# Kernel optimization log

Hardware: AMD Instinct MI355X
Metric: run time of the kernel (lower is better)

## Reference

```python
import jax, jax.numpy as jnp
import numpy as np

B, T, Z, X, R, HT, HO = 512, 256, 128, 64, 1024, 1024, 1024


def _linear(x, w, b):
    return x @ w.T + b


def _loc_scale(x, p):
    # p = (gate_ih_w, gate_ih_b, gate_hz_w, gate_hz_b,
    #      prop_ih_w, prop_ih_b, prop_hz_w, prop_hz_b,
    #      loc_w, loc_b, scale_w, scale_b)
    (g_ih_w, g_ih_b, g_hz_w, g_hz_b,
     p_ih_w, p_ih_b, p_hz_w, p_hz_b,
     l_w, l_b, s_w, s_b) = p
    gate = jax.nn.sigmoid(_linear(jax.nn.relu(_linear(x, g_ih_w, g_ih_b)), g_hz_w, g_hz_b))
    proposed = _linear(jax.nn.relu(_linear(x, p_ih_w, p_ih_b)), p_hz_w, p_hz_b)
    loc = (1.0 - gate) * _linear(x, l_w, l_b) + gate * proposed
    scale = jax.nn.softplus(_linear(jax.nn.relu(proposed), s_w, s_b))
    return loc, scale


def _gru_cell(x, h, w_ih, b_ih, w_hh, b_hh):
    # torch GRUCell: gates ordered (r, z, n)
    gi = x @ w_ih.T + b_ih
    gh = h @ w_hh.T + b_hh
    i_r, i_z, i_n = jnp.split(gi, 3, axis=-1)
    h_r, h_z, h_n = jnp.split(gh, 3, axis=-1)
    r = jax.nn.sigmoid(i_r + h_r)
    z = jax.nn.sigmoid(i_z + h_z)
    n = jnp.tanh(i_n + r * h_n)
    return (1.0 - z) * n + z * h


def _mk_linear(key, out_dim, in_dim, std=0.02):
    kw, kb = jax.random.split(key)
    w = jax.random.normal(kw, (out_dim, in_dim), jnp.float32) * std
    b = jnp.zeros((out_dim,), jnp.float32)
    return w, b


def setup_inputs() -> dict:
    key = jax.random.key(0)
    ks = jax.random.split(key, 20)
    inp = {}
    inp['mini_batch'] = jax.random.normal(ks[0], (B, T, X), jnp.float32)
    inp['eps'] = jax.random.normal(ks[1], (B, T, Z), jnp.float32)
    inp['z_0'] = jnp.zeros((Z,), jnp.float32)
    inp['h_0'] = jnp.zeros((R,), jnp.float32)
    # GRUCell params
    inp['gru_w_ih'], inp['gru_b_ih'] = _mk_linear(ks[2], 3 * R, Z)
    inp['gru_w_hh'], inp['gru_b_hh'] = _mk_linear(ks[3], 3 * R, R)
    # trans LocScaleTransformer: in=R, out=Z, hidden=HT
    inp['t_gate_ih_w'], inp['t_gate_ih_b'] = _mk_linear(ks[4], HT, R)
    inp['t_gate_hz_w'], inp['t_gate_hz_b'] = _mk_linear(ks[5], Z, HT)
    inp['t_prop_ih_w'], inp['t_prop_ih_b'] = _mk_linear(ks[6], HT, R)
    inp['t_prop_hz_w'], inp['t_prop_hz_b'] = _mk_linear(ks[7], Z, HT)
    inp['t_loc_w'], inp['t_loc_b'] = _mk_linear(ks[8], Z, R)
    inp['t_scale_w'], inp['t_scale_b'] = _mk_linear(ks[9], Z, Z)
    # obs LocScaleTransformer: in=Z, out=X, hidden=HO
    inp['o_gate_ih_w'], inp['o_gate_ih_b'] = _mk_linear(ks[10], HO, Z)
    inp['o_gate_hz_w'], inp['o_gate_hz_b'] = _mk_linear(ks[11], X, HO)
    inp['o_prop_ih_w'], inp['o_prop_ih_b'] = _mk_linear(ks[12], HO, Z)
    inp['o_prop_hz_w'], inp['o_prop_hz_b'] = _mk_linear(ks[13], X, HO)
    inp['o_loc_w'], inp['o_loc_b'] = _mk_linear(ks[14], X, Z)
    inp['o_scale_w'], inp['o_scale_b'] = _mk_linear(ks[15], X, X)
    return inp


def reference(mini_batch, eps, z_0, h_0,
              gru_w_ih, gru_b_ih, gru_w_hh, gru_b_hh,
              t_gate_ih_w, t_gate_ih_b, t_gate_hz_w, t_gate_hz_b,
              t_prop_ih_w, t_prop_ih_b, t_prop_hz_w, t_prop_hz_b,
              t_loc_w, t_loc_b, t_scale_w, t_scale_b,
              o_gate_ih_w, o_gate_ih_b, o_gate_hz_w, o_gate_hz_b,
              o_prop_ih_w, o_prop_ih_b, o_prop_hz_w, o_prop_hz_b,
              o_loc_w, o_loc_b, o_scale_w, o_scale_b):
    b = mini_batch.shape[0]
    trans_p = (t_gate_ih_w, t_gate_ih_b, t_gate_hz_w, t_gate_hz_b,
               t_prop_ih_w, t_prop_ih_b, t_prop_hz_w, t_prop_hz_b,
               t_loc_w, t_loc_b, t_scale_w, t_scale_b)
    obs_p = (o_gate_ih_w, o_gate_ih_b, o_gate_hz_w, o_gate_hz_b,
             o_prop_ih_w, o_prop_ih_b, o_prop_hz_w, o_prop_hz_b,
             o_loc_w, o_loc_b, o_scale_w, o_scale_b)

    z_prev = jnp.broadcast_to(z_0, (b, z_0.shape[0]))
    h_prev = jnp.broadcast_to(h_0, (b, h_0.shape[0]))

    def step(carry, eps_t):
        z_p, h_p = carry
        rnn_out = _gru_cell(z_p, h_p, gru_w_ih, gru_b_ih, gru_w_hh, gru_b_hh)
        z_loc, z_scale = _loc_scale(rnn_out, trans_p)
        z_t = z_loc + z_scale * eps_t  # reparameterized Normal sample
        x_loc, x_scale = _loc_scale(z_t, obs_p)
        return (z_t, rnn_out), jnp.concatenate([x_loc, x_scale], axis=-1)

    # scan over time: eps -> [T, B, Z]
    _, out = jax.lax.scan(step, (z_prev, h_prev), eps.transpose(1, 0, 2))
    return out.transpose(1, 0, 2)  # [B, T, 2*X]
```

## Files before the change

kernel.cpp:

```cpp
#include <hip/hip_runtime.h>
#include <math.h>


typedef unsigned short u16;
typedef unsigned long long u64;
typedef __bf16 bf16x8 __attribute__((ext_vector_type(8)));
typedef u16    u16x8  __attribute__((ext_vector_type(8)));
typedef float  f32x4  __attribute__((ext_vector_type(4)));

#define DI __device__ __forceinline__
#define LDS_STRIDE 72

DI u16  f2b(float f){ union{float f; unsigned u;} c; c.f = f;
                      return (u16)((c.u + 0x7fffu + ((c.u>>16)&1u))>>16); }
DI float b2f(u16 x){ union{unsigned u; float f;} c; c.u = ((unsigned)x)<<16; return c.f; }
DI float sigm (float x){ return 1.f/(1.f+expf(-x)); }
DI float softp(float x){ return (x>15.f)? x : log1pf(expf(x)); }

DI f32x4 mfma16(bf16x8 a, bf16x8 b, f32x4 c){
  return __builtin_amdgcn_mfma_f32_16x16x32_bf16(a,b,c,0,0,0);
}
DI bf16x8 ldw8b(const u16* __restrict__ g){
  return __builtin_bit_cast(bf16x8, *(const u16x8*)g);
}
DI bf16x8 ldfragS(const u16* l, int row, int ko, int stride){
  return __builtin_bit_cast(bf16x8, *(const u16x8*)(l + row*stride + ko));
}
DI bf16x8 ldfrag(const u16* l, int row, int ko){ return ldfragS(l, row, ko, LDS_STRIDE); }

DI u64 ldc64(const void* p){
  return __hip_atomic_load((const u64*)p, __ATOMIC_RELAXED, __HIP_MEMORY_SCOPE_AGENT);
}
DI u16x8 ldc128(const u16* g){
  union{u64 q[2]; u16x8 v;} u; u.q[0] = ldc64(g); u.q[1] = ldc64(g + 4); return u.v;
}
DI u16 ldc16(const u16* p){
  return __hip_atomic_load(p, __ATOMIC_RELAXED, __HIP_MEMORY_SCOPE_AGENT);
}
DI void stc16(u16* p, u16 v){
  __hip_atomic_store(p, v, __ATOMIC_RELAXED, __HIP_MEMORY_SCOPE_AGENT);
}
DI float ldc32f(const float* p){
  unsigned u = __hip_atomic_load((const unsigned*)p, __ATOMIC_RELAXED, __HIP_MEMORY_SCOPE_AGENT);
  union{unsigned u; float f;} c; c.u = u; return c.f;
}
DI void stc32f(float* p, float v){
  union{float f; unsigned u;} c; c.f = v;
  __hip_atomic_store((unsigned*)p, c.u, __ATOMIC_RELAXED, __HIP_MEMORY_SCOPE_AGENT);
}

DI void gsync(unsigned* bar, unsigned bi, int blk){
  __syncthreads();
  if(threadIdx.x == 0){
    unsigned v = __hip_atomic_fetch_add(bar + (blk & 7)*32, 1u,
                   __ATOMIC_RELAXED, __HIP_MEMORY_SCOPE_AGENT);
    if(v == bi*64u + 63u){
      unsigned r = __hip_atomic_fetch_add(bar + 256, 1u,
                     __ATOMIC_RELAXED, __HIP_MEMORY_SCOPE_AGENT);
      if(r == bi*8u + 7u)
        __hip_atomic_store(bar + 288, bi + 1u,
                           __ATOMIC_RELAXED, __HIP_MEMORY_SCOPE_AGENT);
    }
    while(__hip_atomic_load(bar + 288, __ATOMIC_RELAXED,
                            __HIP_MEMORY_SCOPE_AGENT) <= bi)
      __builtin_amdgcn_s_sleep(4);
  }
  asm volatile("" ::: "memory");
  __syncthreads();
}

__global__ __launch_bounds__(256) void k_cvt(const float* __restrict__ s,
                                             u16* __restrict__ d){
  int i = (blockIdx.x*256 + threadIdx.x)*8;
  f32x4 p0 = *(const f32x4*)(s+i), p1 = *(const f32x4*)(s+i+4);
  u16x8 o;
  o[0]=f2b(p0[0]); o[1]=f2b(p0[1]); o[2]=f2b(p0[2]); o[3]=f2b(p0[3]);
  o[4]=f2b(p1[0]); o[5]=f2b(p1[1]); o[6]=f2b(p1[2]); o[7]=f2b(p1[3]);
  *(u16x8*)(d+i) = o;
}

__global__ __launch_bounds__(256) void k_init(u16* __restrict__ hb,
                                              u16* __restrict__ zb,
                                              const float* __restrict__ h0,
                                              const float* __restrict__ z0){
  int idx = blockIdx.x*256 + threadIdx.x;
  hb[idx] = f2b(h0[idx & 1023]);
  if(idx < 512*128) zb[idx] = f2b(z0[idx & 127]);
}

__global__ void k_bzero(unsigned* b){ b[threadIdx.x] = 0u; b[threadIdx.x+256] = 0u; }

struct SeqP {
  const float *eps, *h0, *z0;
  const float *gbih, *gbhh, *tgb, *tpb, *tlb, *tghzb, *tphzb, *tsb;
  const u16 *wih, *whh, *tgw, *tpw, *tlw, *tghzw, *tphzw, *tsw;
  float *out, *GP;
  u16 *Hbuf, *hb16, *zb16;
  unsigned *bar;
};

DI void mlp_tile(const u16* __restrict__ A,
                 const u16* __restrict__ W,
                 const float* __restrict__ bias, int act,
                 u16* __restrict__ Cb,
                 u16* smem, int tid)
{
  const int lane=tid&63, w=tid>>6, l16=lane&15, quad=lane>>4, wm=w>>1, wn=w&1;
  const int ar=tid>>3, ac=(tid&7)*8, br=tid>>2, bc=(tid&3)*16;
  f32x4 acc[2] = {};
  u16x8 a0,a1,a2,a3,u0,u1,u2,u3,v0,v1,v2,v3;
#define MT_ISSUE(ra,ru,rv,is) do{ \
    ra = ldc128(A + (size_t)ar*1024 + (is)*64 + ac); \
    ru = *(const u16x8*)(W + (size_t)br*1024 + (is)*64 + bc); \
    rv = *(const u16x8*)(W + (size_t)br*1024 + (is)*64 + bc + 8); \
  }while(0)
#define MT_STEP(ra,ru,rv,it,nx) do{ \
    u16* b_ = smem + ((it)&1)*6912; \
    *(u16x8*)(b_ + ar*LDS_STRIDE + ac) = ra; \
    *(u16x8*)(b_ + 2304 + br*LDS_STRIDE + bc) = ru; \
    *(u16x8*)(b_ + 2304 + br*LDS_STRIDE + bc + 8) = rv; \
    asm volatile("s_waitcnt lgkmcnt(0)" ::: "memory"); \
    __builtin_amdgcn_s_barrier(); \
    __builtin_amdgcn_sched_barrier(0); \
    if((nx) < 16) MT_ISSUE(ra,ru,rv,(nx)); \
    _Pragma("unroll") \
    for(int kc=0;kc<2;kc++){ \
      int ko = kc*32 + quad*8; \
      bf16x8 aa = ldfrag(b_, wm*16 + l16, ko); \
      bf16x8 q0 = ldfrag(b_ + 2304, wn*32 + l16, ko); \
      bf16x8 q1 = ldfrag(b_ + 2304, wn*32 + 16 + l16, ko); \
      acc[0] = mfma16(aa,q0,acc[0]); \
      acc[1] = mfma16(aa,q1,acc[1]); \
    } \
  }while(0)
  MT_ISSUE(a0,u0,v0,0); MT_ISSUE(a1,u1,v1,1);
  MT_ISSUE(a2,u2,v2,2); MT_ISSUE(a3,u3,v3,3);
#pragma unroll 1
  for(int ib=0; ib<16; ib+=4){
    MT_STEP(a0,u0,v0, ib+0, ib+4);
    MT_STEP(a1,u1,v1, ib+1, ib+5);
    MT_STEP(a2,u2,v2, ib+2, ib+6);
    MT_STEP(a3,u3,v3, ib+3, ib+7);
  }
#undef MT_ISSUE
#undef MT_STEP
  __syncthreads();
#pragma unroll
  for(int nf=0; nf<2; nf++)
#pragma unroll
  for(int i=0; i<4; i++){
    int m  = wm*16 + quad*4 + i;
    int cl = wn*32 + nf*16 + l16;
    float v = acc[nf][i] + bias[cl];
    if(act) v = fmaxf(v, 0.f);
    stc16(&Cb[(size_t)m*2176 + cl], f2b(v));
  }
}

__global__ __launch_bounds__(256, 2) void k_seq(SeqP p)
{
  __shared__ u16 smem[18432];
  const int blk  = blockIdx.x;
  const int tid  = threadIdx.x;
  const int lane = tid & 63, w = tid >> 6;
  const int l16  = lane & 15, quad = lane >> 4;
  const int wm   = w >> 1, wn = w & 1;
  const int ar   = tid >> 3, ac = (tid & 7) * 8;

  const int p1m0 = (blk >> 5) * 32;
  const int p1n0 = (blk & 31) * 32;
  const int p1n  = p1n0 + wn*16 + l16;
  f32x4 hreg;
  { float h0v = p.h0[p1n]; hreg[0]=h0v; hreg[1]=h0v; hreg[2]=h0v; hreg[3]=h0v; }

  unsigned bi = 0;

#pragma unroll 1
  for(int t = 0; t < 256; t++){
    const u16* hbi = p.hb16 + (size_t)(t&1)*524288;
    u16*       hbo = p.hb16 + (size_t)((t+1)&1)*524288;

    {
      f32x4 acc[4] = {};
      u16x8 a0,a1,a2, w00,w01,w02, w10,w11,w12, w20,w21,w22;
#define P1_ISSUE(ra,r0,r1,r2,is) do{ \
      const u16 *A_, *W_; int ld_, k0_; \
      if((is) < 2){ A_ = p.zb16 + (size_t)p1m0*128;  W_ = p.wih; ld_=128;  k0_=(is)*64; } \
      else        { A_ = hbi    + (size_t)p1m0*1024; W_ = p.whh; ld_=1024; k0_=((is)-2)*64; } \
      ra = ldc128(A_ + (size_t)ar*ld_ + k0_ + ac); \
      r0 = *(const u16x8*)(W_ + (size_t)(p1n0 + ar)*ld_        + k0_ + ac); \
      r1 = *(const u16x8*)(W_ + (size_t)(1024 + p1n0 + ar)*ld_ + k0_ + ac); \
      r2 = *(const u16x8*)(W_ + (size_t)(2048 + p1n0 + ar)*ld_ + k0_ + ac); \
    }while(0)
#define P1_STEP(ra,r0,r1,r2,it,nx) do{ \
      u16* b_ = smem + ((it)&1)*9216; \
      *(u16x8*)(b_ + ar*LDS_STRIDE + ac) = ra; \
      *(u16x8*)(b_ + 2304 + ar*LDS_STRIDE + ac) = r0; \
      *(u16x8*)(b_ + 4608 + ar*LDS_STRIDE + ac) = r1; \
      *(u16x8*)(b_ + 6912 + ar*LDS_STRIDE + ac) = r2; \
      asm volatile("s_waitcnt lgkmcnt(0)" ::: "memory"); \
      __builtin_amdgcn_s_barrier(); \
      __builtin_amdgcn_sched_barrier(0); \
      if((nx) < 18) P1_ISSUE(ra,r0,r1,r2,(nx)); \
      const int ai3_ = ((it) < 2) ? 2 : 3; \
      _Pragma("unroll") \
      for(int kc=0;kc<2;kc++){ \
        int ko = kc*32 + quad*8; \
        bf16x8 aa  = ldfrag(b_, wm*16 + l16, ko); \
        bf16x8 b0v = ldfrag(b_ + 2304, wn*16 + l16, ko); \
        bf16x8 b1v = ldfrag(b_ + 4608, wn*16 + l16, ko); \
        bf16x8 b2v = ldfrag(b_ + 6912, wn*16 + l16, ko); \
        acc[0]    = mfma16(aa,b0v,acc[0]); \
        acc[1]    = mfma16(aa,b1v,acc[1]); \
        acc[ai3_] = mfma16(aa,b2v,acc[ai3_]); \
      } \
    }while(0)
      P1_ISSUE(a0,w00,w01,w02,0);
      P1_ISSUE(a1,w10,w11,w12,1);
      P1_ISSUE(a2,w20,w21,w22,2);
#pragma unroll 1
      for(int ib=0; ib<18; ib+=3){
        P1_STEP(a0,w00,w01,w02, ib+0, ib+3);
        P1_STEP(a1,w10,w11,w12, ib+1, ib+4);
        P1_STEP(a2,w20,w21,w22, ib+2, ib+5);
      }
#undef P1_ISSUE
#undef P1_STEP
      __syncthreads();
#pragma unroll
      for(int i=0; i<4; i++){
        int m = p1m0 + wm*16 + quad*4 + i;
        int n = p1n;
        float r  = sigm (acc[0][i] + p.gbih[n]      + p.gbhh[n]);
        float z  = sigm (acc[1][i] + p.gbih[n+1024] + p.gbhh[n+1024]);
        float nn = tanhf(acc[2][i] + p.gbih[n+2048]
                         + r*(acc[3][i] + p.gbhh[n+2048]));
        float hv = (1.f-z)*nn + z*hreg[i];
        hreg[i] = hv;
        stc16(&hbo[(size_t)m*1024 + n], f2b(hv));
      }
    }
    gsync(p.bar, bi++, blk);

    {
      const int m0 = (blk >> 5) * 32;
      const int n0 = (blk & 31) * 64;
      const u16* W; const float* bias;
      if(n0 < 1024){ W = p.tgw + (size_t)n0*1024;        bias = p.tgb + n0; }
      else         { W = p.tpw + (size_t)(n0-1024)*1024; bias = p.tpb + (n0-1024); }
      mlp_tile(hbo + (size_t)m0*1024, W, bias, 1,
               p.Hbuf + (size_t)m0*2176 + n0, smem, tid);
    }
    gsync(p.bar, bi++, blk);

    if(blk < 128){
      const int m0 = (blk >> 3) * 32, n0 = (blk & 7) * 32;
      const int reg1 = (n0 >= 128);
      const u16*  A = p.Hbuf + (size_t)m0*2176 + (reg1 ? 1024 : 0);
      const u16*  W = reg1 ? p.tphzw + (size_t)(n0-128)*1024
                           : p.tghzw + (size_t)n0*1024;
      const float* bias = reg1 ? p.tphzb + (n0-128) : p.tghzb + n0;
      f32x4 acc3 = {};
      u16x8 a0,a1,a2,a3, q0,q1,q2,q3;
#define P3_ISSUE(ra,rw,is) do{ \
      ra = ldc128(A + (size_t)ar*2176 + (is)*64 + ac); \
      rw = *(const u16x8*)(W + (size_t)ar*1024 + (is)*64 + ac); \
    }while(0)
#define P3_STEP(ra,rw,it,nx) do{ \
      u16* b_ = smem + ((it)&1)*4608; \
      *(u16x8*)(b_ + ar*LDS_STRIDE + ac) = ra; \
      *(u16x8*)(b_ + 2304 + ar*LDS_STRIDE + ac) = rw; \
      asm volatile("s_waitcnt lgkmcnt(0)" ::: "memory"); \
      __builtin_amdgcn_s_barrier(); \
      __builtin_amdgcn_sched_barrier(0); \
      if((nx) < 16) P3_ISSUE(ra,rw,(nx)); \
      _Pragma("unroll") \
      for(int kc=0;kc<2;kc++){ \
        int ko = kc*32 + quad*8; \
        acc3 = mfma16(ldfrag(b_, wm*16 + l16, ko), \
                      ldfrag(b_ + 2304, wn*16 + l16, ko), acc3); \
      } \
    }while(0)
      P3_ISSUE(a0,q0,0); P3_ISSUE(a1,q1,1); P3_ISSUE(a2,q2,2); P3_ISSUE(a3,q3,3);
#pragma unroll 1
      for(int ib=0; ib<16; ib+=4){
        P3_STEP(a0,q0, ib+0, ib+4);
        P3_STEP(a1,q1, ib+1, ib+5);
        P3_STEP(a2,q2, ib+2, ib+6);
        P3_STEP(a3,q3, ib+3, ib+7);
      }
#undef P3_ISSUE
#undef P3_STEP
      __syncthreads();
#pragma unroll
      for(int i=0; i<4; i++){
        int m  = m0 + wm*16 + quad*4 + i;
        int cl = wn*16 + l16;
        stc32f(&p.GP[(size_t)m*256 + n0 + cl], acc3[i] + bias[cl]);
      }
    } else if(blk < 160){
      const int idx = blk - 128;
      const int m0  = (idx & 15) * 32;
      const int n0l = 2048 + (idx >> 4) * 64;
      mlp_tile(hbo + (size_t)m0*1024, p.tlw + (size_t)(n0l-2048)*1024,
               p.tlb + (n0l-2048), 0,
               p.Hbuf + (size_t)m0*2176 + n0l, smem, tid);
    }
    gsync(p.bar, bi++, blk);

    if(blk < 64){
      const int m0 = (blk >> 1) * 16, n0 = (blk & 1) * 64;
      u16* lp = smem;
      {
        int r = tid >> 4, c = (tid & 15) * 8;
        const float* src = p.GP + (size_t)(m0+r)*256 + 128 + c;
        union{u64 q; float f[2];} q0,q1,q2,q3;
        q0.q = ldc64(src);   q1.q = ldc64(src+2);
        q2.q = ldc64(src+4); q3.q = ldc64(src+6);
        u16x8 o;
        o[0]=f2b(fmaxf(q0.f[0],0.f)); o[1]=f2b(fmaxf(q0.f[1],0.f));
        o[2]=f2b(fmaxf(q1.f[0],0.f)); o[3]=f2b(fmaxf(q1.f[1],0.f));
        o[4]=f2b(fmaxf(q2.f[0],0.f)); o[5]=f2b(fmaxf(q2.f[1],0.f));
        o[6]=f2b(fmaxf(q3.f[0],0.f)); o[7]=f2b(fmaxf(q3.f[1],0.f));
        *(u16x8*)(lp + r*136 + c) = o;
      }
      __syncthreads();
      f32x4 acc4 = {};
      const int col = n0 + w*16 + l16;
#pragma unroll
      for(int kc=0; kc<4; kc++){
        int ko = kc*32 + quad*8;
        acc4 = mfma16(ldfragS(lp, l16, ko, 136),
                      ldw8b(p.tsw + (size_t)col*128 + ko), acc4);
      }
#pragma unroll
      for(int i=0; i<4; i++){
        int gm = m0 + quad*4 + i;
        float zs  = softp(acc4[i] + p.tsb[col]);
        float g   = sigm(ldc32f(&p.GP[(size_t)gm*256 + col]));
        float pv  = ldc32f(&p.GP[(size_t)gm*256 + 128 + col]);
        float loc = b2f(ldc16(&p.Hbuf[(size_t)gm*2176 + 2048 + col]));
        float zl  = (1.f-g)*loc + g*pv;
        float e   = p.eps[(size_t)gm*32768 + (size_t)t*128 + col];
        float zv  = zl + zs*e;
        p.out[(size_t)gm*32768 + (size_t)t*128 + col] = zv;
        stc16(&p.zb16[(size_t)gm*128 + col], f2b(zv));
      }
    }
    gsync(p.bar, bi++, blk);
  }
}

#define LH_S 520
__global__ __launch_bounds__(256) void k_obs(
  const u16* __restrict__ ogw,   const float* __restrict__ ogb,
  const u16* __restrict__ oghzw, const float* __restrict__ oghzb,
  const u16* __restrict__ opw,   const float* __restrict__ opb,
  const u16* __restrict__ ophzw, const float* __restrict__ ophzb,
  const u16* __restrict__ olw,   const float* __restrict__ olb,
  const u16* __restrict__ osw,   const float* __restrict__ osb,
  float* __restrict__ out)
{
  __shared__ u16 lz[32*136];
  __shared__ u16 lh[32*LH_S];
  __shared__ u16 lp[32*72];
  const int r0 = blockIdx.x*32;
  const int t  = r0 >> 9, b0 = r0 & 511;
  const int tid = threadIdx.x;
  const int lane = tid & 63, w = tid>>6, l16 = lane&15, quad = lane>>4;

#pragma unroll
  for(int i=0;i<2;i++){
    int ch = tid + i*256;
    int r = ch>>4, c = (ch&15)*8;
    const float* src = out + (size_t)(b0+r)*32768 + (size_t)t*128 + c;
    f32x4 p0 = *(const f32x4*)src, p1 = *(const f32x4*)(src+4);
    u16x8 o;
    o[0]=f2b(p0[0]); o[1]=f2b(p0[1]); o[2]=f2b(p0[2]); o[3]=f2b(p0[3]);
    o[4]=f2b(p1[0]); o[5]=f2b(p1[1]); o[6]=f2b(p1[2]); o[7]=f2b(p1[3]);
    *(u16x8*)(lz + r*136 + c) = o;
  }
  __syncthreads();

  f32x4 accp[2] = {}, accg[2] = {};
  const int col = w*16 + l16;

#pragma unroll 1
  for(int ph=0; ph<2; ph++){
    const u16* hw = ph ? ogw   : opw;
    const float* hb = ph ? ogb : opb;
    const u16* zw = ph ? oghzw : ophzw;
    f32x4* acc2    = ph ? accg : accp;
#pragma unroll 1
    for(int c2=0; c2<2; c2++){
      __syncthreads();
      for(int nt = w; nt < 32; nt += 4){
        int n = c2*512 + nt*16 + l16;
#pragma unroll
        for(int mi=0; mi<2; mi++){
          f32x4 a = {};
#pragma unroll
          for(int kc=0;kc<4;kc++){
            int ko = kc*32 + quad*8;
            a = mfma16(ldfragS(lz, mi*16+l16, ko, 136),
                       ldw8b(hw + (size_t)n*128 + ko), a);
          }
          float bias = hb[n];
#pragma unroll
          for(int i=0;i<4;i++)
            lh[(mi*16+quad*4+i)*LH_S + nt*16 + l16] = f2b(fmaxf(a[i]+bias, 0.f));
        }
      }
      __syncthreads();
#pragma unroll
      for(int mi=0;mi<2;mi++){
        f32x4 a = acc2[mi];
        for(int kc=0;kc<16;kc++){
          int ko = kc*32 + quad*8;
          a = mfma16(ldfragS(lh, mi*16+l16, ko, LH_S),
                     ldw8b(zw + (size_t)col*1024 + c2*512 + ko), a);
        }
        acc2[mi] = a;
      }
    }
    if(ph==0){
      float bias = ophzb[col];
#pragma unroll
      for(int mi=0;mi<2;mi++)
#pragma unroll
      for(int i=0;i<4;i++){
        float pv = accp[mi][i] + bias;
        accp[mi][i] = pv;
        lp[(mi*16+quad*4+i)*72 + col] = f2b(fmaxf(pv, 0.f));
      }
    }
  }

  f32x4 accl[2]={}, accs[2]={};
#pragma unroll
  for(int mi=0;mi<2;mi++){
#pragma unroll
    for(int kc=0;kc<4;kc++){
      int ko=kc*32+quad*8;
      accl[mi]=mfma16(ldfragS(lz,mi*16+l16,ko,136),
                      ldw8b(olw + (size_t)col*128 + ko), accl[mi]);
    }
#pragma unroll
    for(int kc=0;kc<2;kc++){
      int ko=kc*32+quad*8;
      accs[mi]=mfma16(ldfragS(lp,mi*16+l16,ko,72),
                      ldw8b(osw + (size_t)col*64 + ko), accs[mi]);
    }
  }
#pragma unroll
  for(int mi=0;mi<2;mi++)
#pragma unroll
  for(int i=0;i<4;i++){
    int r = mi*16 + quad*4 + i;
    float g  = sigm(accg[mi][i] + oghzb[col]);
    float pv = accp[mi][i];
    float lc = accl[mi][i] + olb[col];
    float xs = softp(accs[mi][i] + osb[col]);
    float xl = (1.f-g)*lc + g*pv;
    size_t o = (size_t)(b0+r)*32768 + (size_t)t*128 + col;
    out[o]      = xl;
    out[o + 64] = xs;
  }
}

extern "C" void kernel_launch(void* const* d_in, const int* in_sizes, int n_in,
                              void* d_out, int out_size, void* d_ws, size_t ws_size,
                              hipStream_t stream)
{
  (void)in_sizes; (void)n_in; (void)out_size; (void)ws_size;
  const float* eps   = (const float*)d_in[1];
  const float* z0    = (const float*)d_in[2];
  const float* h0    = (const float*)d_in[3];
  const float* gwih  = (const float*)d_in[4];  const float* gbih  = (const float*)d_in[5];
  const float* gwhh  = (const float*)d_in[6];  const float* gbhh  = (const float*)d_in[7];
  const float* tgw   = (const float*)d_in[8];  const float* tgb   = (const float*)d_in[9];
  const float* tghzw = (const float*)d_in[10]; const float* tghzb = (const float*)d_in[11];
  const float* tpw   = (const float*)d_in[12]; const float* tpb   = (const float*)d_in[13];
  const float* tphzw = (const float*)d_in[14]; const float* tphzb = (const float*)d_in[15];
  const float* tlw   = (const float*)d_in[16]; const float* tlb   = (const float*)d_in[17];
  const float* tsw   = (const float*)d_in[18]; const float* tsb   = (const float*)d_in[19];
  const float* ogw   = (const float*)d_in[20]; const float* ogb   = (const float*)d_in[21];
  const float* oghzw = (const float*)d_in[22]; const float* oghzb = (const float*)d_in[23];
  const float* opw   = (const float*)d_in[24]; const float* opb   = (const float*)d_in[25];
  const float* ophzw = (const float*)d_in[26]; const float* ophzb = (const float*)d_in[27];
  const float* olw   = (const float*)d_in[28]; const float* olb   = (const float*)d_in[29];
  const float* osw   = (const float*)d_in[30]; const float* osb   = (const float*)d_in[31];
  float* out = (float*)d_out;

  char* ws = (char*)d_ws;
  size_t off = 0;
  u16*   Hbuf = (u16*)  (ws + off); off += (size_t)512*2176*2;
  float* GP   = (float*)(ws + off); off += (size_t)512*256*4;
  u16*   hb16 = (u16*)  (ws + off); off += (size_t)2*512*1024*2;
  u16*   zb16 = (u16*)  (ws + off); off += (size_t)512*128*2;
  u16* wc_gwih  = (u16*)(ws + off); off += (size_t)3072*128 *2;
  u16* wc_gwhh  = (u16*)(ws + off); off += (size_t)3072*1024*2;
  u16* wc_tgw   = (u16*)(ws + off); off += (size_t)1024*1024*2;
  u16* wc_tpw   = (u16*)(ws + off); off += (size_t)1024*1024*2;
  u16* wc_tlw   = (u16*)(ws + off); off += (size_t)128*1024 *2;
  u16* wc_tghzw = (u16*)(ws + off); off += (size_t)128*1024 *2;
  u16* wc_tphzw = (u16*)(ws + off); off += (size_t)128*1024 *2;
  u16* wc_tsw   = (u16*)(ws + off); off += (size_t)128*128  *2;
  u16* wc_ogw   = (u16*)(ws + off); off += (size_t)1024*128 *2;
  u16* wc_opw   = (u16*)(ws + off); off += (size_t)1024*128 *2;
  u16* wc_oghzw = (u16*)(ws + off); off += (size_t)64*1024  *2;
  u16* wc_ophzw = (u16*)(ws + off); off += (size_t)64*1024  *2;
  u16* wc_olw   = (u16*)(ws + off); off += (size_t)64*128   *2;
  u16* wc_osw   = (u16*)(ws + off); off += (size_t)64*64    *2;
  unsigned* bar = (unsigned*)(ws + off); off += 2048;

  #define CVT(src, dst, n) k_cvt<<<(n)/2048, 256, 0, stream>>>((src), (dst))
  CVT(gwih,  wc_gwih,  3072*128);
  CVT(gwhh,  wc_gwhh,  3072*1024);
  CVT(tgw,   wc_tgw,   1024*1024);
  CVT(tpw,   wc_tpw,   1024*1024);
  CVT(tlw,   wc_tlw,   128*1024);
  CVT(tghzw, wc_tghzw, 128*1024);
  CVT(tphzw, wc_tphzw, 128*1024);
  CVT(tsw,   wc_tsw,   128*128);
  CVT(ogw,   wc_ogw,   1024*128);
  CVT(opw,   wc_opw,   1024*128);
  CVT(oghzw, wc_oghzw, 64*1024);
  CVT(ophzw, wc_ophzw, 64*1024);
  CVT(olw,   wc_olw,   64*128);
  CVT(osw,   wc_osw,   64*64);
  #undef CVT
  k_init <<<2048, 256, 0, stream>>>(hb16, zb16, h0, z0);
  k_bzero<<<1, 256, 0, stream>>>(bar);

  SeqP sp;
  sp.eps = eps; sp.h0 = h0; sp.z0 = z0;
  sp.gbih = gbih; sp.gbhh = gbhh;
  sp.tgb = tgb; sp.tpb = tpb; sp.tlb = tlb;
  sp.tghzb = tghzb; sp.tphzb = tphzb; sp.tsb = tsb;
  sp.wih = wc_gwih; sp.whh = wc_gwhh;
  sp.tgw = wc_tgw; sp.tpw = wc_tpw; sp.tlw = wc_tlw;
  sp.tghzw = wc_tghzw; sp.tphzw = wc_tphzw; sp.tsw = wc_tsw;
  sp.out = out; sp.GP = GP;
  sp.Hbuf = Hbuf; sp.hb16 = hb16; sp.zb16 = zb16;
  sp.bar = bar;
  k_seq<<<512, 256, 0, stream>>>(sp);

  k_obs<<<4096, 256, 0, stream>>>(wc_ogw, ogb, wc_oghzw, oghzb,
                                  wc_opw, opb, wc_ophzw, ophzb,
                                  wc_olw, olb, wc_osw, osb, out);
}
```

Measured before the change: 10.77 ms.

## Replace grid-wide barrier with per-batch-group flag synchronization

The global atomic barrier across all 512 blocks is replaced by independent barriers for 16 groups of 32 blocks. Each group owns 32 batch rows. Work in every phase is remapped so a group only touches its own rows, which makes the groups' recurrences independent. Each block writes a per-block u16 step flag, and 32 threads spin on the group's flags. This is meant to cut barrier latency and global atomic contention, and it lets groups drift apart in time. The cost is relying on relaxed flag ordering for data visibility.

```diff
diff --git a/kernel.cpp b/kernel.cpp
--- a/kernel.cpp
+++ b/kernel.cpp
@@ -49,21 +49,14 @@
   __hip_atomic_store((unsigned*)p, c.u, __ATOMIC_RELAXED, __HIP_MEMORY_SCOPE_AGENT);
 }
 
-DI void gsync(unsigned* bar, unsigned bi, int blk){
+DI void csync(u16* cf, unsigned s, int lblk){
   __syncthreads();
-  if(threadIdx.x == 0){
-    unsigned v = __hip_atomic_fetch_add(bar + (blk & 7)*32, 1u,
-                   __ATOMIC_RELAXED, __HIP_MEMORY_SCOPE_AGENT);
-    if(v == bi*64u + 63u){
-      unsigned r = __hip_atomic_fetch_add(bar + 256, 1u,
-                     __ATOMIC_RELAXED, __HIP_MEMORY_SCOPE_AGENT);
-      if(r == bi*8u + 7u)
-        __hip_atomic_store(bar + 288, bi + 1u,
-                           __ATOMIC_RELAXED, __HIP_MEMORY_SCOPE_AGENT);
-    }
-    while(__hip_atomic_load(bar + 288, __ATOMIC_RELAXED,
-                            __HIP_MEMORY_SCOPE_AGENT) <= bi)
-      __builtin_amdgcn_s_sleep(4);
+  if(threadIdx.x == 0)
+    __hip_atomic_store(cf + lblk, (u16)s, __ATOMIC_RELAXED, __HIP_MEMORY_SCOPE_AGENT);
+  if(threadIdx.x < 32){
+    while((unsigned)__hip_atomic_load(cf + threadIdx.x, __ATOMIC_RELAXED,
+                                      __HIP_MEMORY_SCOPE_AGENT) < s)
+      __builtin_amdgcn_s_sleep(1);
   }
   asm volatile("" ::: "memory");
   __syncthreads();
@@ -96,7 +89,7 @@
   const u16 *wih, *whh, *tgw, *tpw, *tlw, *tghzw, *tphzw, *tsw;
   float *out, *GP;
   u16 *Hbuf, *hb16, *zb16;
-  unsigned *bar;
+  u16 *flags;
 };
 
 DI void mlp_tile(const u16* __restrict__ A,
@@ -162,18 +155,21 @@
   __shared__ u16 smem[18432];
   const int blk  = blockIdx.x;
   const int tid  = threadIdx.x;
+  const int g    = blk >> 5;
+  const int lblk = blk & 31;
+  u16* cf = p.flags + g*64;
   const int lane = tid & 63, w = tid >> 6;
   const int l16  = lane & 15, quad = lane >> 4;
   const int wm   = w >> 1, wn = w & 1;
   const int ar   = tid >> 3, ac = (tid & 7) * 8;
 
-  const int p1m0 = (blk >> 5) * 32;
-  const int p1n0 = (blk & 31) * 32;
+  const int p1m0 = g * 32;
+  const int p1n0 = lblk * 32;
   const int p1n  = p1n0 + wn*16 + l16;
   f32x4 hreg;
   { float h0v = p.h0[p1n]; hreg[0]=h0v; hreg[1]=h0v; hreg[2]=h0v; hreg[3]=h0v; }
 
-  unsigned bi = 0;
+  unsigned s = 0;
 
 #pragma unroll 1
   for(int t = 0; t < 256; t++){
@@ -240,21 +236,21 @@
         stc16(&hbo[(size_t)m*1024 + n], f2b(hv));
       }
     }
-    gsync(p.bar, bi++, blk);
+    csync(cf, ++s, lblk);
 
     {
-      const int m0 = (blk >> 5) * 32;
-      const int n0 = (blk & 31) * 64;
+      const int m0 = g * 32;
+      const int n0 = lblk * 64;
       const u16* W; const float* bias;
       if(n0 < 1024){ W = p.tgw + (size_t)n0*1024;        bias = p.tgb + n0; }
       else         { W = p.tpw + (size_t)(n0-1024)*1024; bias = p.tpb + (n0-1024); }
       mlp_tile(hbo + (size_t)m0*1024, W, bias, 1,
                p.Hbuf + (size_t)m0*2176 + n0, smem, tid);
     }
-    gsync(p.bar, bi++, blk);
-
-    if(blk < 128){
-      const int m0 = (blk >> 3) * 32, n0 = (blk & 7) * 32;
+    csync(cf, ++s, lblk);
+
+    if(lblk < 8){
+      const int m0 = g * 32, n0 = lblk * 32;
       const int reg1 = (n0 >= 128);
       const u16*  A = p.Hbuf + (size_t)m0*2176 + (reg1 ? 1024 : 0);
       const u16*  W = reg1 ? p.tphzw + (size_t)(n0-128)*1024
@@ -298,18 +294,17 @@
         int cl = wn*16 + l16;
         stc32f(&p.GP[(size_t)m*256 + n0 + cl], acc3[i] + bias[cl]);
       }
-    } else if(blk < 160){
-      const int idx = blk - 128;
-      const int m0  = (idx & 15) * 32;
-      const int n0l = 2048 + (idx >> 4) * 64;
+    } else if(lblk < 10){
+      const int m0  = g * 32;
+      const int n0l = 2048 + (lblk - 8) * 64;
       mlp_tile(hbo + (size_t)m0*1024, p.tlw + (size_t)(n0l-2048)*1024,
                p.tlb + (n0l-2048), 0,
                p.Hbuf + (size_t)m0*2176 + n0l, smem, tid);
     }
-    gsync(p.bar, bi++, blk);
-
-    if(blk < 64){
-      const int m0 = (blk >> 1) * 16, n0 = (blk & 1) * 64;
+    csync(cf, ++s, lblk);
+
+    if(lblk < 4){
+      const int m0 = g*32 + (lblk >> 1)*16, n0 = (lblk & 1)*64;
       u16* lp = smem;
       {
         int r = tid >> 4, c = (tid & 15) * 8;
@@ -337,17 +332,17 @@
       for(int i=0; i<4; i++){
         int gm = m0 + quad*4 + i;
         float zs  = softp(acc4[i] + p.tsb[col]);
-        float g   = sigm(ldc32f(&p.GP[(size_t)gm*256 + col]));
+        float gt  = sigm(ldc32f(&p.GP[(size_t)gm*256 + col]));
         float pv  = ldc32f(&p.GP[(size_t)gm*256 + 128 + col]);
         float loc = b2f(ldc16(&p.Hbuf[(size_t)gm*2176 + 2048 + col]));
-        float zl  = (1.f-g)*loc + g*pv;
+        float zl  = (1.f-gt)*loc + gt*pv;
         float e   = p.eps[(size_t)gm*32768 + (size_t)t*128 + col];
         float zv  = zl + zs*e;
         p.out[(size_t)gm*32768 + (size_t)t*128 + col] = zv;
         stc16(&p.zb16[(size_t)gm*128 + col], f2b(zv));
       }
     }
-    gsync(p.bar, bi++, blk);
+    csync(cf, ++s, lblk);
   }
 }
 
@@ -543,7 +538,7 @@
   sp.tghzw = wc_tghzw; sp.tphzw = wc_tphzw; sp.tsw = wc_tsw;
   sp.out = out; sp.GP = GP;
   sp.Hbuf = Hbuf; sp.hb16 = hb16; sp.zb16 = zb16;
-  sp.bar = bar;
+  sp.flags = (u16*)bar;
   k_seq<<<512, 256, 0, stream>>>(sp);
 
   k_obs<<<4096, 256, 0, stream>>>(wc_ogw, ogb, wc_oghzw, oghzb,
```

New measurement: 11.81 ms. 9.7% more time.
